# Kernel tuning notes

Hardware: AMD Instinct MI355X
Metric: run time of the kernel (lower is better)

Reference implementation:

```python
import jax, jax.numpy as jnp
import numpy as np

B, T, I, H = 64, 512, 512, 1024

def setup_inputs() -> dict:
    key = jax.random.key(0)
    k1, k2, k3, k4 = jax.random.split(key, 4)
    s_ih = 1.0 / np.sqrt(I)
    s_hh = 1.0 / np.sqrt(H)
    return {
        "input_seq": jax.random.normal(k1, (B, T, I), dtype=jnp.float32),
        "W_ih": jax.random.uniform(k2, (H, I), dtype=jnp.float32, minval=-s_ih, maxval=s_ih),
        "b_ih": jax.random.uniform(k3, (H,), dtype=jnp.float32, minval=-s_ih, maxval=s_ih),
        "W_hh": jax.random.uniform(k4, (H, H), dtype=jnp.float32, minval=-s_hh, maxval=s_hh),
    }

def reference(input_seq, W_ih, b_ih, W_hh):
    # Precompute the input projection for all timesteps in one big GEMM.
    # xW: [B, T, H]
    xW = jnp.einsum('bti,hi->bth', input_seq, W_ih) + b_ih
    h0 = jnp.zeros((input_seq.shape[0], W_hh.shape[0]), dtype=input_seq.dtype)

    def step(h, x_t):  # x_t: [B, H]
        h_new = jnp.tanh(x_t + h @ W_hh.T)
        return h_new, h_new

    _, ys = jax.lax.scan(step, h0, jnp.swapaxes(xW, 0, 1))  # ys: [T, B, H]
    return jnp.swapaxes(ys, 0, 1)  # [B, T, H]
```

## Files before the change

### kernel.cpp

```cpp
#include <hip/hip_runtime.h>
#include <math.h>

#define T_SEQ 512
#define B_SZ  64
#define I_DIM 512
#define H_DIM 1024

typedef __attribute__((ext_vector_type(8))) short     short8;
typedef __attribute__((ext_vector_type(4))) float     f32x4;

#define HROW   1032
#define HPLANE (8 * HROW)
#define RED_OFF HPLANE
#define RECUR_LDS_BYTES 148096
#define RING 4

#define XKP 40

__device__ __forceinline__ unsigned short f2bf_rn(float f) {
    unsigned u = __float_as_uint(f);
    unsigned r = u + 0x7fffu + ((u >> 16) & 1u);
    return (unsigned short)(r >> 16);
}
__device__ __forceinline__ float bf2f(unsigned short s) {
    return __uint_as_float(((unsigned)s) << 16);
}

__global__ __launch_bounds__(256) void wsplit_kernel(
    const float* __restrict__ W, unsigned short* __restrict__ Whi,
    unsigned short* __restrict__ Wlo, int n)
{
    int i = blockIdx.x * 256 + threadIdx.x;
    if (i < n) {
        float w = W[i];
        unsigned short hi = f2bf_rn(w);
        Whi[i] = hi;
        Wlo[i] = f2bf_rn(w - bf2f(hi));
    }
}

__global__ __launch_bounds__(256) void xw_mfma_kernel(
    const float* __restrict__ input,
    const unsigned short* __restrict__ Whi,
    const unsigned short* __restrict__ Wlo,
    const float* __restrict__ b_ih,
    float* __restrict__ xw,
    int t0, int ntch)
{
    __shared__ short xhi[128 * XKP];
    __shared__ short xlo[128 * XKP];
    __shared__ short whi[128 * XKP];
    __shared__ short wlo[128 * XKP];

    const int tid = threadIdx.x;
    const int per = 64 * ntch;
    const int grp = blockIdx.x % per;
    const int hch = blockIdx.x / per;
    const int b   = grp & 63;
    const int tch = grp >> 6;
    const int n0  = hch * 128;
    const int w   = tid >> 6;
    const int l   = tid & 63;

    const float* xsrc = input + ((size_t)b * T_SEQ + t0 + tch * 128) * I_DIM;
    const unsigned short* whsrc = Whi + (size_t)n0 * I_DIM;
    const unsigned short* wlsrc = Wlo + (size_t)n0 * I_DIM;

    f32x4 acc[8][2] = {};

    const int srow = tid >> 1;
    const int skq  = (tid & 1) * 16;

    for (int kt = 0; kt < I_DIM; kt += 32) {
        {
            const float* p = xsrc + (size_t)srow * I_DIM + kt + skq;
            union S8 { short s[8]; short8 v; };
            S8 h0, h1, l0, l1;
            #pragma unroll
            for (int i = 0; i < 8; ++i) {
                float f = p[i];
                unsigned short hh = f2bf_rn(f);
                h0.s[i] = (short)hh; l0.s[i] = (short)f2bf_rn(f - bf2f(hh));
            }
            #pragma unroll
            for (int i = 0; i < 8; ++i) {
                float f = p[8 + i];
                unsigned short hh = f2bf_rn(f);
                h1.s[i] = (short)hh; l1.s[i] = (short)f2bf_rn(f - bf2f(hh));
            }
            *(short8*)&xhi[srow * XKP + skq]     = h0.v;
            *(short8*)&xhi[srow * XKP + skq + 8] = h1.v;
            *(short8*)&xlo[srow * XKP + skq]     = l0.v;
            *(short8*)&xlo[srow * XKP + skq + 8] = l1.v;
        }
        {
            const unsigned short* ph = whsrc + (size_t)srow * I_DIM + kt + skq;
            const unsigned short* pl = wlsrc + (size_t)srow * I_DIM + kt + skq;
            *(short8*)&whi[srow * XKP + skq]     = *(const short8*)(ph);
            *(short8*)&whi[srow * XKP + skq + 8] = *(const short8*)(ph + 8);
            *(short8*)&wlo[srow * XKP + skq]     = *(const short8*)(pl);
            *(short8*)&wlo[srow * XKP + skq + 8] = *(const short8*)(pl + 8);
        }
        __syncthreads();

        short8 bh[2], bl[2];
        #pragma unroll
        for (int ni = 0; ni < 2; ++ni) {
            int brow = w * 32 + ni * 16 + (l & 15);
            bh[ni] = *(const short8*)&whi[brow * XKP + (l >> 4) * 8];
            bl[ni] = *(const short8*)&wlo[brow * XKP + (l >> 4) * 8];
        }
        #pragma unroll
        for (int mi = 0; mi < 8; ++mi) {
            int arow = mi * 16 + (l & 15);
            short8 ah = *(const short8*)&xhi[arow * XKP + (l >> 4) * 8];
            short8 al = *(const short8*)&xlo[arow * XKP + (l >> 4) * 8];
            #pragma unroll
            for (int ni = 0; ni < 2; ++ni) {
                acc[mi][ni] = __builtin_amdgcn_mfma_f32_16x16x32_bf16(ah, bh[ni], acc[mi][ni], 0, 0, 0);
                acc[mi][ni] = __builtin_amdgcn_mfma_f32_16x16x32_bf16(al, bh[ni], acc[mi][ni], 0, 0, 0);
                acc[mi][ni] = __builtin_amdgcn_mfma_f32_16x16x32_bf16(ah, bl[ni], acc[mi][ni], 0, 0, 0);
            }
        }
        __syncthreads();
    }

    const int tb = tch * 128;
    #pragma unroll
    for (int ni = 0; ni < 2; ++ni) {
        int col = n0 + w * 32 + ni * 16 + (l & 15);
        float bias = b_ih[col];
        #pragma unroll
        for (int mi = 0; mi < 8; ++mi)
            #pragma unroll
            for (int r = 0; r < 4; ++r) {
                int s = tb + mi * 16 + (l >> 4) * 4 + r;
                xw[((size_t)s * B_SZ + b) * H_DIM + col] = acc[mi][ni][r] + bias;
            }
    }
}

__global__ __launch_bounds__(256) void xw_gemm_kernel(
    const float* __restrict__ input, const float* __restrict__ W_ih,
    const float* __restrict__ b_ih, float* __restrict__ xw,
    int t0)
{
    __shared__ float Ash[32 * 68];
    __shared__ float Bsh[32 * 68];

    const int bm  = blockIdx.x >> 4;
    const int bn  = blockIdx.x & 15;
    const int tid = threadIdx.x;
    const int tx  = tid & 15;
    const int ty  = tid >> 4;

    const int t = t0 + bm;
    const float* Abase = input + (size_t)t * I_DIM;
    const float* Bbase = W_ih + (size_t)(bn * 64) * I_DIM;

    float acc[4][4] = {};

    for (int kt = 0; kt < I_DIM; kt += 32) {
        #pragma unroll
        for (int p = 0; p < 2; ++p) {
            int idx = tid + p * 256;
            int row = idx >> 3;
            int c4  = (idx & 7) << 2;
            float4 a = *(const float4*)(Abase + (size_t)row * (T_SEQ * I_DIM) + kt + c4);
            float4 b = *(const float4*)(Bbase + (size_t)row * I_DIM + kt + c4);
            Ash[(c4 + 0) * 68 + row] = a.x; Ash[(c4 + 1) * 68 + row] = a.y;
            Ash[(c4 + 2) * 68 + row] = a.z; Ash[(c4 + 3) * 68 + row] = a.w;
            Bsh[(c4 + 0) * 68 + row] = b.x; Bsh[(c4 + 1) * 68 + row] = b.y;
            Bsh[(c4 + 2) * 68 + row] = b.z; Bsh[(c4 + 3) * 68 + row] = b.w;
        }
        __syncthreads();
        #pragma unroll
        for (int k = 0; k < 32; ++k) {
            float4 a4 = *(const float4*)&Ash[k * 68 + ty * 4];
            float4 b4 = *(const float4*)&Bsh[k * 68 + tx * 4];
            float av[4] = {a4.x, a4.y, a4.z, a4.w};
            float bv[4] = {b4.x, b4.y, b4.z, b4.w};
            #pragma unroll
            for (int i = 0; i < 4; ++i)
                #pragma unroll
                for (int j = 0; j < 4; ++j)
                    acc[i][j] += av[i] * bv[j];
        }
        __syncthreads();
    }

    const int ncol = bn * 64 + tx * 4;
    float4 bias = *(const float4*)(b_ih + ncol);
    #pragma unroll
    for (int i = 0; i < 4; ++i) {
        int b = ty * 4 + i;
        float4 v;
        v.x = acc[i][0] + bias.x; v.y = acc[i][1] + bias.y;
        v.z = acc[i][2] + bias.z; v.w = acc[i][3] + bias.w;
        *(float4*)(xw + ((size_t)bm * B_SZ + b) * H_DIM + ncol) = v;
    }
}

__global__ __launch_bounds__(256, 1) void elman_recur_kernel(
    const float* __restrict__ xw,
    const unsigned short* __restrict__ Whi,
    const unsigned short* __restrict__ Wlo,
    unsigned int* __restrict__ hbuf,
    unsigned int* __restrict__ sent,
    float* __restrict__ out,
    int t0, int tc)
{
    extern __shared__ __align__(16) short smem[];
    short* hA  = smem;
    float* red = (float*)(smem + RED_OFF);

    const int tid = threadIdx.x;
    const int bg  = blockIdx.x & 7;
    const int js  = blockIdx.x >> 3;
    const int w   = tid >> 6;
    const int l   = tid & 63;
    const int b   = tid & 7;
    const int jl  = tid >> 3;
    const int jg  = js * 32 + jl;
    const int bgl = bg * 8 + b;

    short8 Bhi[2][8], Blo[2][8];
    {
        const int n  = l & 15;
        const int kb = (l >> 4) * 8;
        #pragma unroll
        for (int t2 = 0; t2 < 2; ++t2) {
            const unsigned short* rhi = Whi + (size_t)(js * 32 + t2 * 16 + n) * H_DIM;
            const unsigned short* rlo = Wlo + (size_t)(js * 32 + t2 * 16 + n) * H_DIM;
            #pragma unroll
            for (int ks = 0; ks < 8; ++ks) {
                int k = w * 256 + ks * 32 + kb;
                Bhi[t2][ks] = *(const short8*)(rhi + k);
                Blo[t2][ks] = *(const short8*)(rlo + k);
            }
        }
    }

    for (int s = 0; s < tc; ++s) {
        const int t = t0 + s;

        float pre = xw[((size_t)s * B_SZ + bgl) * H_DIM + jg];

        if (t > 0) {
            const unsigned tagw = (unsigned)(t - 1);
            const unsigned long long* grp = (const unsigned long long*)
                (hbuf + (size_t)((t - 1) & (RING - 1)) * B_SZ * H_DIM
                      + (size_t)bg * 8 * H_DIM);

            {
                const unsigned want = (unsigned)t;
                const unsigned* sgrp = sent + bg * 32 + w * 8;
                for (;;) {
                    unsigned sv = __hip_atomic_load(sgrp + (l & 7), __ATOMIC_RELAXED,
                                                    __HIP_MEMORY_SCOPE_AGENT);
                    if (__all((int)(sv >= want))) break;
                }
            }

            unsigned long long v[8][2];
            for (;;) {
                #pragma unroll
                for (int p = 0; p < 8; ++p) {
                    #pragma unroll
                    for (int i = 0; i < 2; ++i)
                        v[p][i] = __hip_atomic_load(grp + p * 512 + w * 128 + i * 64 + l,
                                                    __ATOMIC_RELAXED,
                                                    __HIP_MEMORY_SCOPE_AGENT);
                }
                int ok = 1;
                #pragma unroll
                for (int p = 0; p < 8; ++p)
                    #pragma unroll
                    for (int i = 0; i < 2; ++i) {
                        ok &= (((unsigned)(v[p][i] >> 16) & 0xffffu) == tagw);
                        ok &= ((unsigned)(v[p][i] >> 48) == tagw);
                    }
                if (__all(ok)) break;
            }

            #pragma unroll
            for (int p = 0; p < 8; ++p)
                #pragma unroll
                for (int i = 0; i < 2; ++i) {
                    int c = w * 256 + i * 128 + l * 2;
                    unsigned lo32 = (unsigned)v[p][i];
                    unsigned hi32 = (unsigned)(v[p][i] >> 32);
                    *(unsigned*)(hA + p * HROW + c) = (lo32 & 0xffffu) | (hi32 << 16);
                }

            f32x4 acc0 = {0.f, 0.f, 0.f, 0.f};
            f32x4 acc1 = {0.f, 0.f, 0.f, 0.f};
            const short* aAb = hA + (l & 7) * HROW + w * 256 + ((l >> 4) * 8);
            #pragma unroll
            for (int ks = 0; ks < 8; ++ks) {
                short8 ah = *(const short8*)(aAb + ks * 32);
                acc0 = __builtin_amdgcn_mfma_f32_16x16x32_bf16(ah, Bhi[0][ks], acc0, 0, 0, 0);
                acc1 = __builtin_amdgcn_mfma_f32_16x16x32_bf16(ah, Bhi[1][ks], acc1, 0, 0, 0);
                acc0 = __builtin_amdgcn_mfma_f32_16x16x32_bf16(ah, Blo[0][ks], acc0, 0, 0, 0);
                acc1 = __builtin_amdgcn_mfma_f32_16x16x32_bf16(ah, Blo[1][ks], acc1, 0, 0, 0);
            }
            *(f32x4*)&red[((w * 2 + 0) * 16 + (l & 15)) * 16 + (l >> 4) * 4] = acc0;
            *(f32x4*)&red[((w * 2 + 1) * 16 + (l & 15)) * 16 + (l >> 4) * 4] = acc1;
            __syncthreads();

            const int tt = jl >> 4, c = jl & 15;
            #pragma unroll
            for (int w2 = 0; w2 < 4; ++w2)
                pre += red[((w2 * 2 + tt) * 16 + c) * 16 + b];
        }

        float hval = tanhf(pre);

        unsigned packed = ((unsigned)t << 16) | (unsigned)f2bf_rn(hval);
        __hip_atomic_store(hbuf + (size_t)(t & (RING - 1)) * B_SZ * H_DIM
                                + (size_t)bgl * H_DIM + jg,
                           packed, __ATOMIC_RELAXED, __HIP_MEMORY_SCOPE_AGENT);
        __builtin_nontemporal_store(hval, out + ((size_t)bgl * T_SEQ + t) * H_DIM + jg);

        __syncthreads();
        if (tid == 0)
            __hip_atomic_store(sent + bg * 32 + js, (unsigned)(t + 1),
                               __ATOMIC_RELAXED, __HIP_MEMORY_SCOPE_AGENT);
    }
}

extern "C" void kernel_launch(void* const* d_in, const int* in_sizes, int n_in,
                              void* d_out, int out_size, void* d_ws, size_t ws_size,
                              hipStream_t stream) {
    (void)in_sizes; (void)n_in; (void)out_size;
    const float* input = (const float*)d_in[0];
    const float* W_ih  = (const float*)d_in[1];
    const float* b_ih  = (const float*)d_in[2];
    const float* W_hh  = (const float*)d_in[3];
    float* out = (float*)d_out;

    char* ws = (char*)d_ws;
    unsigned int*   hbuf   = (unsigned int*)ws;
    unsigned int*   sent   = (unsigned int*)(ws + (1 << 20));
    unsigned short* Whh_hi = (unsigned short*)(ws + (1 << 20) + (64 << 10));
    unsigned short* Whh_lo = (unsigned short*)(ws + (3 << 20) + (64 << 10));
    unsigned short* Wih_hi = (unsigned short*)(ws + (5 << 20) + (64 << 10));
    unsigned short* Wih_lo = (unsigned short*)(ws + (6 << 20) + (64 << 10));
    const size_t    xw_off = (size_t)(7 << 20) + (64 << 10);
    float*          xwbuf  = (float*)(ws + xw_off);

    const size_t slice_bytes = (size_t)B_SZ * H_DIM * sizeof(float);
    size_t avail = ws_size > xw_off ? ws_size - xw_off : 0;
    int Tc = (int)(avail / slice_bytes);
    if (Tc > T_SEQ) Tc = T_SEQ;
    bool mfma_xw = (Tc >= 128);
    if (mfma_xw) Tc &= ~127;
    if (Tc < 1)  Tc = 1;

    hipFuncSetAttribute((const void*)elman_recur_kernel,
                        hipFuncAttributeMaxDynamicSharedMemorySize,
                        RECUR_LDS_BYTES);

    hipMemsetAsync(sent, 0, 8 * 32 * sizeof(unsigned int), stream);

    wsplit_kernel<<<dim3(4096), dim3(256), 0, stream>>>(
        W_hh, Whh_hi, Whh_lo, H_DIM * H_DIM);
    wsplit_kernel<<<dim3(2048), dim3(256), 0, stream>>>(
        W_ih, Wih_hi, Wih_lo, H_DIM * I_DIM);

    for (int t0 = 0; t0 < T_SEQ; t0 += Tc) {
        int tc = (T_SEQ - t0 < Tc) ? (T_SEQ - t0) : Tc;

        if (mfma_xw && (tc % 128) == 0) {
            int ntch = tc / 128;
            xw_mfma_kernel<<<dim3(8 * 64 * ntch), dim3(256), 0, stream>>>(
                input, Wih_hi, Wih_lo, b_ih, xwbuf, t0, ntch);
        } else {
            xw_gemm_kernel<<<dim3((unsigned)tc * 16), dim3(256), 0, stream>>>(
                input, W_ih, b_ih, xwbuf, t0);
        }

        elman_recur_kernel<<<dim3(256), dim3(256), RECUR_LDS_BYTES, stream>>>(
            xwbuf, Whh_hi, Whh_lo, hbuf, sent, out, t0, tc);
    }
}
```

Measured before the change: 1.601 ms.

## Drop sentinel flags and sync on tagged hidden-state data with per-plane polling

Removes the separate per-block `sent` counter handshake, which cost a global flag poll, a trailing block barrier and a flag store every step. Consumers now poll the tagged hidden-state words directly and re-load only the batch planes still stale. The reduction scratch is double-buffered by step parity, so the end-of-step `__syncthreads` can go, and the LDS row pitch of the h tile changes. The ring-buffer safety now relies only on data tags and the implicit lockstep of the dependency chain. Polling payload words directly may add memory traffic while waiting.

```diff
diff --git a/kernel.cpp b/kernel.cpp
--- a/kernel.cpp
+++ b/kernel.cpp
@@ -9,7 +9,7 @@
 typedef __attribute__((ext_vector_type(8))) short     short8;
 typedef __attribute__((ext_vector_type(4))) float     f32x4;
 
-#define HROW   1032
+#define HROW   1040
 #define HPLANE (8 * HROW)
 #define RED_OFF HPLANE
 #define RECUR_LDS_BYTES 148096
@@ -206,13 +206,12 @@
     const unsigned short* __restrict__ Whi,
     const unsigned short* __restrict__ Wlo,
     unsigned int* __restrict__ hbuf,
-    unsigned int* __restrict__ sent,
     float* __restrict__ out,
     int t0, int tc)
 {
     extern __shared__ __align__(16) short smem[];
-    short* hA  = smem;
-    float* red = (float*)(smem + RED_OFF);
+    short* hA   = smem;
+    float* redb = (float*)(smem + RED_OFF);
 
     const int tid = threadIdx.x;
     const int bg  = blockIdx.x & 7;
@@ -243,6 +242,7 @@
 
     for (int s = 0; s < tc; ++s) {
         const int t = t0 + s;
+        float* red = redb + (s & 1) * (4 * 2 * 16 * 16);
 
         float pre = xw[((size_t)s * B_SZ + bgl) * H_DIM + jg];
 
@@ -252,36 +252,31 @@
                 (hbuf + (size_t)((t - 1) & (RING - 1)) * B_SZ * H_DIM
                       + (size_t)bg * 8 * H_DIM);
 
-            {
-                const unsigned want = (unsigned)t;
-                const unsigned* sgrp = sent + bg * 32 + w * 8;
-                for (;;) {
-                    unsigned sv = __hip_atomic_load(sgrp + (l & 7), __ATOMIC_RELAXED,
-                                                    __HIP_MEMORY_SCOPE_AGENT);
-                    if (__all((int)(sv >= want))) break;
-                }
-            }
-
             unsigned long long v[8][2];
-            for (;;) {
+            unsigned stale = 0xffu;
+            do {
                 #pragma unroll
                 for (int p = 0; p < 8; ++p) {
-                    #pragma unroll
-                    for (int i = 0; i < 2; ++i)
-                        v[p][i] = __hip_atomic_load(grp + p * 512 + w * 128 + i * 64 + l,
+                    if (stale & (1u << p)) {
+                        v[p][0] = __hip_atomic_load(grp + p * 512 + w * 128 + l,
                                                     __ATOMIC_RELAXED,
                                                     __HIP_MEMORY_SCOPE_AGENT);
+                        v[p][1] = __hip_atomic_load(grp + p * 512 + w * 128 + 64 + l,
+                                                    __ATOMIC_RELAXED,
+                                                    __HIP_MEMORY_SCOPE_AGENT);
+                    }
                 }
-                int ok = 1;
                 #pragma unroll
-                for (int p = 0; p < 8; ++p)
-                    #pragma unroll
-                    for (int i = 0; i < 2; ++i) {
-                        ok &= (((unsigned)(v[p][i] >> 16) & 0xffffu) == tagw);
-                        ok &= ((unsigned)(v[p][i] >> 48) == tagw);
+                for (int p = 0; p < 8; ++p) {
+                    if (stale & (1u << p)) {
+                        int ok = (((unsigned)(v[p][0] >> 16) & 0xffffu) == tagw);
+                        ok &= ((unsigned)(v[p][0] >> 48) == tagw);
+                        ok &= (((unsigned)(v[p][1] >> 16) & 0xffffu) == tagw);
+                        ok &= ((unsigned)(v[p][1] >> 48) == tagw);
+                        if (__all(ok)) stale &= ~(1u << p);
                     }
-                if (__all(ok)) break;
-            }
+                }
+            } while (stale);
 
             #pragma unroll
             for (int p = 0; p < 8; ++p)
@@ -321,11 +316,6 @@
                                 + (size_t)bgl * H_DIM + jg,
                            packed, __ATOMIC_RELAXED, __HIP_MEMORY_SCOPE_AGENT);
         __builtin_nontemporal_store(hval, out + ((size_t)bgl * T_SEQ + t) * H_DIM + jg);
-
-        __syncthreads();
-        if (tid == 0)
-            __hip_atomic_store(sent + bg * 32 + js, (unsigned)(t + 1),
-                               __ATOMIC_RELAXED, __HIP_MEMORY_SCOPE_AGENT);
     }
 }
 
@@ -341,7 +331,6 @@
 
     char* ws = (char*)d_ws;
     unsigned int*   hbuf   = (unsigned int*)ws;
-    unsigned int*   sent   = (unsigned int*)(ws + (1 << 20));
     unsigned short* Whh_hi = (unsigned short*)(ws + (1 << 20) + (64 << 10));
     unsigned short* Whh_lo = (unsigned short*)(ws + (3 << 20) + (64 << 10));
     unsigned short* Wih_hi = (unsigned short*)(ws + (5 << 20) + (64 << 10));
@@ -361,8 +350,6 @@
                         hipFuncAttributeMaxDynamicSharedMemorySize,
                         RECUR_LDS_BYTES);
 
-    hipMemsetAsync(sent, 0, 8 * 32 * sizeof(unsigned int), stream);
-
     wsplit_kernel<<<dim3(4096), dim3(256), 0, stream>>>(
         W_hh, Whh_hi, Whh_lo, H_DIM * H_DIM);
     wsplit_kernel<<<dim3(2048), dim3(256), 0, stream>>>(
@@ -381,6 +368,6 @@
         }
 
         elman_recur_kernel<<<dim3(256), dim3(256), RECUR_LDS_BYTES, stream>>>(
-            xwbuf, Whh_hi, Whh_lo, hbuf, sent, out, t0, tc);
-    }
-}
+            xwbuf, Whh_hi, Whh_lo, hbuf, out, t0, tc);
+    }
+}
```

Measured after the change: 2.155 ms. +34.6%, slower.

## Pack bf16 hidden-state pairs and drop per-element tag validation in recurrence exchange

Applied to the files above, without the earlier changes.

Each 32-bit word of the hidden-state ring buffer now holds two bf16 values instead of one bf16 plus a timestep tag. A lane shuffle pairs neighbouring outputs so half the lanes do the store. Readers no longer spin re-checking tags on every element; they rely only on the per-block `sent` counters before one load pass, which halves exchange traffic and removes the validation loop. The trade-off is that correctness now depends on the relaxed data stores being visible once the relaxed counter update is seen, with no fence between them. The LDS row stride is also widened, presumably to change bank-conflict behaviour on the copy into LDS.

```diff
diff --git a/kernel.cpp b/kernel.cpp
--- a/kernel.cpp
+++ b/kernel.cpp
@@ -9,7 +9,7 @@
 typedef __attribute__((ext_vector_type(8))) short     short8;
 typedef __attribute__((ext_vector_type(4))) float     f32x4;
 
-#define HROW   1032
+#define HROW   1040
 #define HPLANE (8 * HROW)
 #define RED_OFF HPLANE
 #define RECUR_LDS_BYTES 148096
@@ -247,11 +247,6 @@
         float pre = xw[((size_t)s * B_SZ + bgl) * H_DIM + jg];
 
         if (t > 0) {
-            const unsigned tagw = (unsigned)(t - 1);
-            const unsigned long long* grp = (const unsigned long long*)
-                (hbuf + (size_t)((t - 1) & (RING - 1)) * B_SZ * H_DIM
-                      + (size_t)bg * 8 * H_DIM);
-
             {
                 const unsigned want = (unsigned)t;
                 const unsigned* sgrp = sent + bg * 32 + w * 8;
@@ -262,36 +257,19 @@
                 }
             }
 
-            unsigned long long v[8][2];
-            for (;;) {
-                #pragma unroll
-                for (int p = 0; p < 8; ++p) {
-                    #pragma unroll
-                    for (int i = 0; i < 2; ++i)
-                        v[p][i] = __hip_atomic_load(grp + p * 512 + w * 128 + i * 64 + l,
-                                                    __ATOMIC_RELAXED,
-                                                    __HIP_MEMORY_SCOPE_AGENT);
-                }
-                int ok = 1;
-                #pragma unroll
-                for (int p = 0; p < 8; ++p)
-                    #pragma unroll
-                    for (int i = 0; i < 2; ++i) {
-                        ok &= (((unsigned)(v[p][i] >> 16) & 0xffffu) == tagw);
-                        ok &= ((unsigned)(v[p][i] >> 48) == tagw);
-                    }
-                if (__all(ok)) break;
-            }
-
+            const unsigned long long* grp = (const unsigned long long*)
+                (hbuf + (size_t)((t - 1) & (RING - 1)) * B_SZ * 512
+                      + (size_t)bg * 8 * 512);
+            unsigned long long v[8];
             #pragma unroll
             for (int p = 0; p < 8; ++p)
-                #pragma unroll
-                for (int i = 0; i < 2; ++i) {
-                    int c = w * 256 + i * 128 + l * 2;
-                    unsigned lo32 = (unsigned)v[p][i];
-                    unsigned hi32 = (unsigned)(v[p][i] >> 32);
-                    *(unsigned*)(hA + p * HROW + c) = (lo32 & 0xffffu) | (hi32 << 16);
-                }
+                v[p] = __hip_atomic_load(grp + p * 256 + w * 64 + l,
+                                         __ATOMIC_RELAXED,
+                                         __HIP_MEMORY_SCOPE_AGENT);
+
+            #pragma unroll
+            for (int p = 0; p < 8; ++p)
+                *(unsigned long long*)(hA + p * HROW + w * 256 + l * 4) = v[p];
 
             f32x4 acc0 = {0.f, 0.f, 0.f, 0.f};
             f32x4 acc1 = {0.f, 0.f, 0.f, 0.f};
@@ -316,10 +294,14 @@
 
         float hval = tanhf(pre);
 
-        unsigned packed = ((unsigned)t << 16) | (unsigned)f2bf_rn(hval);
-        __hip_atomic_store(hbuf + (size_t)(t & (RING - 1)) * B_SZ * H_DIM
-                                + (size_t)bgl * H_DIM + jg,
-                           packed, __ATOMIC_RELAXED, __HIP_MEMORY_SCOPE_AGENT);
+        unsigned hb = (unsigned)f2bf_rn(hval);
+        unsigned pb = (unsigned)__shfl_down((int)hb, 8, 64);
+        if (((l >> 3) & 1) == 0) {
+            unsigned packed = hb | (pb << 16);
+            __hip_atomic_store(hbuf + (size_t)(t & (RING - 1)) * B_SZ * 512
+                                    + (size_t)bgl * 512 + (js * 16 + (jl >> 1)),
+                               packed, __ATOMIC_RELAXED, __HIP_MEMORY_SCOPE_AGENT);
+        }
         __builtin_nontemporal_store(hval, out + ((size_t)bgl * T_SEQ + t) * H_DIM + jg);
 
         __syncthreads();
```

Result: faster. 1.283 ms (-19.8%).
